# Performance work log

Hardware: AMD Instinct MI355X
Metric: run time of the kernel (lower is better)

## Reference

```python
import jax, jax.numpy as jnp
import numpy as np

LN_EPS = 1e-5

def setup_inputs() -> dict:
    key = jax.random.key(0)
    k1, k2, k3 = jax.random.split(key, 3)
    L, B, D = 2048, 8, 1024
    x = jax.random.normal(k1, (L, B, D), dtype=jnp.float32)
    c = jnp.zeros((B, D), dtype=jnp.float32)
    W = jax.random.normal(k2, (D, 3 * D), dtype=jnp.float32) * 0.02
    # bias init from _init_bias: u-bias 0, f-bias 0.5, r-bias 0
    b = jnp.concatenate([jnp.zeros(D), jnp.full((D,), 0.5), jnp.zeros(D)]).astype(jnp.float32)
    gamma = jnp.ones((D,), dtype=jnp.float32)
    beta = jnp.zeros((D,), dtype=jnp.float32)
    return {"x": x, "c": c, "W": W, "b": b, "gamma": gamma, "beta": beta}

def reference(x, c, W, b, gamma, beta):
    # LayerNorm over last dim
    mu = jnp.mean(x, axis=-1, keepdims=True)
    var = jnp.mean(jnp.square(x - mu), axis=-1, keepdims=True)
    x_norm = (x - mu) * jax.lax.rsqrt(var + LN_EPS) * gamma + beta
    # Fused u/f/r projection: [L,B,3D]
    ufr = jnp.einsum('lbd,de->lbe', x_norm, W) + b
    u, f, r = jnp.split(ufr, 3, axis=-1)
    f_gate = jax.nn.sigmoid(f)
    r_gate = jax.nn.sigmoid(r)
    # Linear recurrence c_t = f_t * c_{t-1} + (1-f_t) * u_t via scan over time
    def step(c_prev, fu):
        f_t, u_t = fu
        c_t = f_t * c_prev + (1.0 - f_t) * u_t
        return c_t, c_t
    last_c, c_stack = jax.lax.scan(step, c, (f_gate, u))
    hs = r_gate * jnp.tanh(c_stack) + (1.0 - r_gate) * x_norm
    return x + hs, last_c
```

## Files before the change

kernel.cpp:

```cpp
#include <hip/hip_runtime.h>
#include <hip/hip_bf16.h>


typedef unsigned short u16;
typedef __bf16 bf16x8 __attribute__((ext_vector_type(8)));
typedef float f32x4 __attribute__((ext_vector_type(4)));

#define L_DIM 2048
#define B_DIM 8
#define D_DIM 1024
#define M_DIM (L_DIM * B_DIM)
#define K_DIM D_DIM
#define N_DIM (3 * D_DIM)
#define NCH 32
#define CLEN (L_DIM / NCH)

__device__ __forceinline__ float bf2f(u16 h) {
    unsigned int u = ((unsigned int)h) << 16;
    float f;
    __builtin_memcpy(&f, &u, 4);
    return f;
}

__device__ __forceinline__ u16 f2bf(float f) {
    unsigned int u;
    __builtin_memcpy(&u, &f, 4);
    u = u + 0x7fff + ((u >> 16) & 1);
    return (u16)(u >> 16);
}

__device__ __forceinline__ void async16(void* lds, const void* g) {
    __builtin_amdgcn_global_load_lds(
        (const __attribute__((address_space(1))) void*)g,
        (__attribute__((address_space(3))) void*)lds, 16, 0, 0);
}

__global__ __launch_bounds__(256) void ln_kernel(const float* __restrict__ x,
                                                 const float* __restrict__ gamma,
                                                 const float* __restrict__ beta,
                                                 u16* __restrict__ xn) {
    int row = blockIdx.x;
    int tid = threadIdx.x;
    const float4* xr = (const float4*)(x + (size_t)row * D_DIM);
    float4 v = xr[tid];
    float s = v.x + v.y + v.z + v.w;
    float q = v.x * v.x + v.y * v.y + v.z * v.z + v.w * v.w;
    #pragma unroll
    for (int off = 32; off; off >>= 1) {
        s += __shfl_down(s, off);
        q += __shfl_down(q, off);
    }
    __shared__ float ss[4], qq[4];
    int lane = tid & 63, wv = tid >> 6;
    if (lane == 0) { ss[wv] = s; qq[wv] = q; }
    __syncthreads();
    s = ss[0] + ss[1] + ss[2] + ss[3];
    q = qq[0] + qq[1] + qq[2] + qq[3];
    float mu = s * (1.0f / D_DIM);
    float var = q * (1.0f / D_DIM) - mu * mu;
    float rs = rsqrtf(var + 1e-5f);
    float4 g = ((const float4*)gamma)[tid];
    float4 bt = ((const float4*)beta)[tid];
    ushort4 o;
    o.x = f2bf((v.x - mu) * rs * g.x + bt.x);
    o.y = f2bf((v.y - mu) * rs * g.y + bt.y);
    o.z = f2bf((v.z - mu) * rs * g.z + bt.z);
    o.w = f2bf((v.w - mu) * rs * g.w + bt.w);
    ((ushort4*)(xn + (size_t)row * D_DIM))[tid] = o;
}

__global__ __launch_bounds__(256) void wt_kernel(const float* __restrict__ W,
                                                 u16* __restrict__ Wt) {
    __shared__ float t[64][65];
    int k0 = blockIdx.x * 64;
    int n0 = blockIdx.y * 64;
    int col = threadIdx.x & 63;
    int rg4 = threadIdx.x >> 6;
    #pragma unroll
    for (int j = 0; j < 16; ++j) {
        int r = rg4 * 16 + j;
        t[r][col] = W[(size_t)(k0 + r) * N_DIM + n0 + col];
    }
    __syncthreads();
    #pragma unroll
    for (int j = 0; j < 16; ++j) {
        int nr = rg4 * 16 + j;
        Wt[(size_t)(n0 + nr) * K_DIM + k0 + col] = f2bf(t[col][nr]);
    }
}

__global__ __launch_bounds__(256) void gemm_kernel(const u16* __restrict__ A,
                                                   const u16* __restrict__ Bt,
                                                   const float* __restrict__ bias,
                                                   u16* __restrict__ uo,
                                                   u16* __restrict__ fo,
                                                   u16* __restrict__ ro) {
    __shared__ char lds[32768];
    char* ldsA = lds;
    char* ldsB = lds + 16384;
    int tid = threadIdx.x;
    int wave = tid >> 6, lane = tid & 63;
    int lm = lane & 15, lg = lane >> 4;
    int m0 = blockIdx.x * 128;
    int n0 = blockIdx.y * 128;
    int wm = wave >> 1, wn = wave & 1;

    f32x4 acc[4][4] = {};

    for (int kt = 0; kt < K_DIM / 64; ++kt) {
        int k0 = kt * 64;
        #pragma unroll
        for (int i = 0; i < 4; ++i) {
            int c = i * 256 + tid;
            int row = c >> 3;
            int colL = (c & 7) ^ (row & 7);
            const u16* ga = A + (size_t)(m0 + row) * K_DIM + k0 + colL * 8;
            async16(ldsA + i * 4096 + wave * 1024, ga);
            const u16* gb = Bt + (size_t)(n0 + row) * K_DIM + k0 + colL * 8;
            async16(ldsB + i * 4096 + wave * 1024, gb);
        }
        __syncthreads();
        #pragma unroll
        for (int kk = 0; kk < 2; ++kk) {
            bf16x8 av[4], bv[4];
            #pragma unroll
            for (int f = 0; f < 4; ++f) {
                int rowA = wm * 64 + f * 16 + lm;
                av[f] = *(const bf16x8*)(ldsA + rowA * 128 + (((kk * 4 + lg) ^ (rowA & 7)) << 4));
                int rowB = wn * 64 + f * 16 + lm;
                bv[f] = *(const bf16x8*)(ldsB + rowB * 128 + (((kk * 4 + lg) ^ (rowB & 7)) << 4));
            }
            #pragma unroll
            for (int fm = 0; fm < 4; ++fm)
                #pragma unroll
                for (int fn = 0; fn < 4; ++fn)
                    acc[fm][fn] = __builtin_amdgcn_mfma_f32_16x16x32_bf16(
                        av[fm], bv[fn], acc[fm][fn], 0, 0, 0);
        }
        __syncthreads();
    }

    int seg = n0 >> 10;
    u16* outp = (seg == 0) ? uo : ((seg == 1) ? fo : ro);
    #pragma unroll
    for (int fn = 0; fn < 4; ++fn) {
        #pragma unroll
        for (int fm = 0; fm < 4; ++fm) {
            int col = n0 + wn * 64 + fn * 16 + lm;
            int cm = col & 1023;
            float bb = bias[col];
            #pragma unroll
            for (int j = 0; j < 4; ++j) {
                int row = m0 + wm * 64 + fm * 16 + lg * 4 + j;
                float val = acc[fm][fn][j] + bb;
                if (seg != 0) val = 1.0f / (1.0f + __expf(-val));
                outp[(size_t)row * D_DIM + cm] = f2bf(val);
            }
        }
    }
}

__global__ __launch_bounds__(256) void scan1_kernel(const u16* __restrict__ fg,
                                                    const u16* __restrict__ u,
                                                    float* __restrict__ Aa,
                                                    float* __restrict__ Ss) {
    int ch = blockIdx.x;
    int bd = (blockIdx.y * 256 + threadIdx.x) * 2;
    int b = bd >> 10, d = bd & 1023;
    float a0 = 1.0f, a1 = 1.0f, s0 = 0.0f, s1 = 0.0f;
    for (int t = ch * CLEN; t < ch * CLEN + CLEN; ++t) {
        size_t idx = ((size_t)(t * B_DIM + b) << 10) + d;
        ushort2 f2 = *(const ushort2*)(fg + idx);
        ushort2 u2 = *(const ushort2*)(u + idx);
        float f0 = bf2f(f2.x), f1 = bf2f(f2.y);
        float v0 = bf2f(u2.x), v1 = bf2f(u2.y);
        s0 = f0 * s0 + (1.0f - f0) * v0;
        s1 = f1 * s1 + (1.0f - f1) * v1;
        a0 *= f0;
        a1 *= f1;
    }
    int o = ch * 8192 + bd;
    *(float2*)(Aa + o) = make_float2(a0, a1);
    *(float2*)(Ss + o) = make_float2(s0, s1);
}

__global__ __launch_bounds__(256) void scan2_kernel(const float* __restrict__ Aa,
                                                    const float* __restrict__ Ss,
                                                    const float* __restrict__ c0,
                                                    float* __restrict__ cs,
                                                    float* __restrict__ lastc) {
    int bd = blockIdx.x * 256 + threadIdx.x;
    float c = c0[bd];
    #pragma unroll 4
    for (int ch = 0; ch < NCH; ++ch) {
        cs[ch * 8192 + bd] = c;
        c = Aa[ch * 8192 + bd] * c + Ss[ch * 8192 + bd];
    }
    lastc[bd] = c;
}

__global__ __launch_bounds__(256) void scan3_kernel(const float* __restrict__ cs,
                                                    const u16* __restrict__ fg,
                                                    const u16* __restrict__ u,
                                                    const u16* __restrict__ rg,
                                                    const u16* __restrict__ xn,
                                                    const float* __restrict__ x,
                                                    float* __restrict__ out) {
    int ch = blockIdx.x;
    int bd = (blockIdx.y * 256 + threadIdx.x) * 2;
    int b = bd >> 10, d = bd & 1023;
    float c0v = cs[ch * 8192 + bd];
    float c1v = cs[ch * 8192 + bd + 1];
    for (int t = ch * CLEN; t < ch * CLEN + CLEN; ++t) {
        size_t idx = ((size_t)(t * B_DIM + b) << 10) + d;
        ushort2 f2 = *(const ushort2*)(fg + idx);
        ushort2 u2 = *(const ushort2*)(u + idx);
        ushort2 r2 = *(const ushort2*)(rg + idx);
        ushort2 n2 = *(const ushort2*)(xn + idx);
        float2 x2 = *(const float2*)(x + idx);
        float f0 = bf2f(f2.x), f1 = bf2f(f2.y);
        float v0 = bf2f(u2.x), v1 = bf2f(u2.y);
        float r0 = bf2f(r2.x), r1 = bf2f(r2.y);
        float n0 = bf2f(n2.x), n1 = bf2f(n2.y);
        c0v = f0 * c0v + (1.0f - f0) * v0;
        c1v = f1 * c1v + (1.0f - f1) * v1;
        float h0 = r0 * tanhf(c0v) + (1.0f - r0) * n0;
        float h1 = r1 * tanhf(c1v) + (1.0f - r1) * n1;
        *(float2*)(out + idx) = make_float2(x2.x + h0, x2.y + h1);
    }
}

extern "C" void kernel_launch(void* const* d_in, const int* in_sizes, int n_in,
                              void* d_out, int out_size, void* d_ws, size_t ws_size,
                              hipStream_t stream) {
    const float* x     = (const float*)d_in[0];
    const float* c0    = (const float*)d_in[1];
    const float* W     = (const float*)d_in[2];
    const float* b     = (const float*)d_in[3];
    const float* gamma = (const float*)d_in[4];
    const float* beta  = (const float*)d_in[5];
    float* out = (float*)d_out;
    float* lastc = out + (size_t)M_DIM * D_DIM;

    char* w = (char*)d_ws;
    u16* xn = (u16*)w;  w += (size_t)M_DIM * D_DIM * 2;
    u16* Wt = (u16*)w;  w += (size_t)N_DIM * K_DIM * 2;
    u16* ug = (u16*)w;  w += (size_t)M_DIM * D_DIM * 2;
    u16* fg = (u16*)w;  w += (size_t)M_DIM * D_DIM * 2;
    u16* rg = (u16*)w;  w += (size_t)M_DIM * D_DIM * 2;
    float* Aa = (float*)w; w += (size_t)NCH * 8192 * 4;
    float* Ss = (float*)w; w += (size_t)NCH * 8192 * 4;
    float* cs = (float*)w; w += (size_t)NCH * 8192 * 4;

    ln_kernel<<<M_DIM, 256, 0, stream>>>(x, gamma, beta, xn);
    wt_kernel<<<dim3(K_DIM / 64, N_DIM / 64), 256, 0, stream>>>(W, Wt);
    gemm_kernel<<<dim3(M_DIM / 128, N_DIM / 128), 256, 0, stream>>>(xn, Wt, b, ug, fg, rg);
    scan1_kernel<<<dim3(NCH, 16), 256, 0, stream>>>(fg, ug, Aa, Ss);
    scan2_kernel<<<32, 256, 0, stream>>>(Aa, Ss, c0, cs, lastc);
    scan3_kernel<<<dim3(NCH, 16), 256, 0, stream>>>(cs, fg, ug, rg, xn, x, out);
}
```

Measured before the change: 239.8 us.

## Rewrite GEMM as 256x256 tile with double-buffered LDS software pipeline

Replaces the 128x128 single-buffered GEMM with a 256x256 tile, 512-thread kernel that double-buffers A and B in 144KB of dynamic LDS. Asynchronous global-to-LDS loads for later k-tiles are interleaved with MFMA phases, using setprio, manual barriers and waitcnt. The goal is to hide load latency and raise data reuse per tile. In exchange it needs a large LDS allocation, limiting occupancy to one block per CU, and relies on fragile hand synchronisation.

```diff
diff --git a/kernel.cpp b/kernel.cpp
--- a/kernel.cpp
+++ b/kernel.cpp
@@ -14,6 +14,12 @@
 #define N_DIM (3 * D_DIM)
 #define NCH 32
 #define CLEN (L_DIM / NCH)
+#define NT (K_DIM / 64)
+
+#define LDS_A 0
+#define LDS_B 65536
+#define LDS_DUMMY 131072
+#define LDS_TOTAL 147456
 
 __device__ __forceinline__ float bf2f(u16 h) {
     unsigned int u = ((unsigned int)h) << 16;
@@ -89,75 +95,148 @@
     }
 }
 
-__global__ __launch_bounds__(256) void gemm_kernel(const u16* __restrict__ A,
-                                                   const u16* __restrict__ Bt,
-                                                   const float* __restrict__ bias,
-                                                   u16* __restrict__ uo,
-                                                   u16* __restrict__ fo,
-                                                   u16* __restrict__ ro) {
-    __shared__ char lds[32768];
-    char* ldsA = lds;
-    char* ldsB = lds + 16384;
-    int tid = threadIdx.x;
-    int wave = tid >> 6, lane = tid & 63;
-    int lm = lane & 15, lg = lane >> 4;
-    int m0 = blockIdx.x * 128;
-    int n0 = blockIdx.y * 128;
-    int wm = wave >> 1, wn = wave & 1;
-
-    f32x4 acc[4][4] = {};
-
-    for (int kt = 0; kt < K_DIM / 64; ++kt) {
-        int k0 = kt * 64;
-        #pragma unroll
-        for (int i = 0; i < 4; ++i) {
-            int c = i * 256 + tid;
-            int row = c >> 3;
-            int colL = (c & 7) ^ (row & 7);
-            const u16* ga = A + (size_t)(m0 + row) * K_DIM + k0 + colL * 8;
-            async16(ldsA + i * 4096 + wave * 1024, ga);
-            const u16* gb = Bt + (size_t)(n0 + row) * K_DIM + k0 + colL * 8;
-            async16(ldsB + i * 4096 + wave * 1024, gb);
-        }
-        __syncthreads();
-        #pragma unroll
-        for (int kk = 0; kk < 2; ++kk) {
-            bf16x8 av[4], bv[4];
-            #pragma unroll
-            for (int f = 0; f < 4; ++f) {
-                int rowA = wm * 64 + f * 16 + lm;
-                av[f] = *(const bf16x8*)(ldsA + rowA * 128 + (((kk * 4 + lg) ^ (rowA & 7)) << 4));
-                int rowB = wn * 64 + f * 16 + lm;
-                bv[f] = *(const bf16x8*)(ldsB + rowB * 128 + (((kk * 4 + lg) ^ (rowB & 7)) << 4));
-            }
-            #pragma unroll
-            for (int fm = 0; fm < 4; ++fm)
-                #pragma unroll
-                for (int fn = 0; fn < 4; ++fn)
-                    acc[fm][fn] = __builtin_amdgcn_mfma_f32_16x16x32_bf16(
-                        av[fm], bv[fn], acc[fm][fn], 0, 0, 0);
-        }
-        __syncthreads();
-    }
+__device__ __forceinline__ void stage_half(const u16* __restrict__ gsrc, int base0,
+                                           int t, int h, char* lds, int ldsOp,
+                                           int tid, int wave) {
+    int tc = (t < NT) ? t : 0;
+    int k0 = tc * 64;
+    char* dst0 = (t < NT) ? (lds + ldsOp + (t & 1) * 32768 + h * 16384)
+                          : (lds + LDS_DUMMY);
+    #pragma unroll
+    for (int s = 0; s < 2; ++s) {
+        int c = s * 512 + tid;
+        int row = h * 128 + (c >> 3);
+        int cc = (c & 7) ^ (row & 7);
+        async16(dst0 + s * 8192 + wave * 1024,
+                gsrc + (size_t)(base0 + row) * K_DIM + k0 + cc * 8);
+    }
+}
+
+__global__ __launch_bounds__(512, 2) void gemm_kernel(const u16* __restrict__ A,
+                                                      const u16* __restrict__ Bt,
+                                                      const float* __restrict__ bias,
+                                                      u16* __restrict__ uo,
+                                                      u16* __restrict__ fo,
+                                                      u16* __restrict__ ro) {
+    extern __shared__ char lds[];
+    const int tid = threadIdx.x;
+    const int wave = tid >> 6, lane = tid & 63;
+    const int lm = lane & 15, lg = lane >> 4;
+    const int wm = wave >> 2, wn = wave & 3;
+    const int m0 = blockIdx.x * 256;
+    const int n0 = blockIdx.y * 256;
+
+    f32x4 acc[8][4] = {};
+    bf16x8 av[4][2], aw[4][2], bv[4][2];
+
+#define LDA(dst, bb, mf0)                                                       \
+    do { _Pragma("unroll")                                                      \
+        for (int q = 0; q < 4; ++q) {                                           \
+            int row_ = wm * 128 + ((mf0) + q) * 16 + lm;                        \
+            const char* p_ = lds + LDS_A + (bb) * 32768 + row_ * 128;           \
+            _Pragma("unroll")                                                   \
+            for (int kk = 0; kk < 2; ++kk)                                      \
+                dst[q][kk] = *(const bf16x8*)(p_ + ((((kk << 2) | lg) ^ (row_ & 7)) << 4)); \
+        } } while (0)
+
+#define LDB(bb, kk)                                                             \
+    do { _Pragma("unroll")                                                      \
+        for (int nf = 0; nf < 4; ++nf) {                                        \
+            int row_ = wn * 64 + nf * 16 + lm;                                  \
+            bv[nf][kk] = *(const bf16x8*)(lds + LDS_B + (bb) * 32768 + row_ * 128 \
+                                          + ((((kk << 2) | lg) ^ (row_ & 7)) << 4)); \
+        } } while (0)
+
+#define MFMA16(r0, afr, kk)                                                     \
+    do { _Pragma("unroll")                                                      \
+        for (int q = 0; q < 4; ++q)                                             \
+            _Pragma("unroll")                                                   \
+            for (int nf = 0; nf < 4; ++nf)                                      \
+                acc[(r0) + q][nf] = __builtin_amdgcn_mfma_f32_16x16x32_bf16(    \
+                    afr[q][kk], bv[nf][kk], acc[(r0) + q][nf], 0, 0, 0);        \
+    } while (0)
+
+#define PH_SYNC()                                                               \
+    do { __builtin_amdgcn_s_barrier();                                          \
+         asm volatile("s_waitcnt lgkmcnt(0)");                                  \
+         __builtin_amdgcn_sched_barrier(0); } while (0)
+
+#define TILE_BODY(t, bb, last)                                                  \
+    do {                                                                        \
+                 \
+        LDA(av, bb, 0);                                                         \
+        LDB(bb, 0);                                                             \
+        stage_half(A, m0, (t) + 1, 0, lds, LDS_A, tid, wave);                   \
+        PH_SYNC();                                                              \
+        __builtin_amdgcn_s_setprio(1);                                          \
+        MFMA16(0, av, 0);                                                       \
+        __builtin_amdgcn_s_setprio(0);                                          \
+        __builtin_amdgcn_s_barrier();                                           \
+                                     \
+        LDB(bb, 1);                                                             \
+        stage_half(A, m0, (t) + 1, 1, lds, LDS_A, tid, wave);                   \
+        PH_SYNC();                                                              \
+        __builtin_amdgcn_s_setprio(1);                                          \
+        MFMA16(0, av, 1);                                                       \
+        __builtin_amdgcn_s_setprio(0);                                          \
+        __builtin_amdgcn_s_barrier();                                           \
+                                   \
+        LDA(aw, bb, 4);                                                         \
+        stage_half(Bt, n0, (t) + 2, 0, lds, LDS_B, tid, wave);                  \
+        PH_SYNC();                                                              \
+        __builtin_amdgcn_s_setprio(1);                                          \
+        MFMA16(4, aw, 0);                                                       \
+        __builtin_amdgcn_s_setprio(0);                                          \
+        __builtin_amdgcn_s_barrier();                                           \
+                         \
+        stage_half(Bt, n0, (t) + 2, 1, lds, LDS_B, tid, wave);                  \
+        __builtin_amdgcn_s_barrier();                                           \
+        __builtin_amdgcn_s_setprio(1);                                          \
+        MFMA16(4, aw, 1);                                                       \
+        __builtin_amdgcn_s_setprio(0);                                          \
+        if (!(last)) asm volatile("s_waitcnt vmcnt(4)" ::: "memory");           \
+        __builtin_amdgcn_s_barrier();                                           \
+    } while (0)
+
+    stage_half(A, m0, 0, 0, lds, LDS_A, tid, wave);
+    stage_half(A, m0, 0, 1, lds, LDS_A, tid, wave);
+    stage_half(Bt, n0, 0, 0, lds, LDS_B, tid, wave);
+    stage_half(Bt, n0, 0, 1, lds, LDS_B, tid, wave);
+    stage_half(Bt, n0, 1, 0, lds, LDS_B, tid, wave);
+    stage_half(Bt, n0, 1, 1, lds, LDS_B, tid, wave);
+    asm volatile("s_waitcnt vmcnt(4)" ::: "memory");
+    __builtin_amdgcn_s_barrier();
+
+    for (int t = 0; t < NT - 2; t += 2) {
+        TILE_BODY(t, 0, 0);
+        TILE_BODY(t + 1, 1, 0);
+    }
+    TILE_BODY(NT - 2, 0, 0);
+    TILE_BODY(NT - 1, 1, 1);
 
     int seg = n0 >> 10;
     u16* outp = (seg == 0) ? uo : ((seg == 1) ? fo : ro);
     #pragma unroll
-    for (int fn = 0; fn < 4; ++fn) {
+    for (int mf = 0; mf < 8; ++mf) {
         #pragma unroll
-        for (int fm = 0; fm < 4; ++fm) {
-            int col = n0 + wn * 64 + fn * 16 + lm;
+        for (int nf = 0; nf < 4; ++nf) {
+            int col = n0 + wn * 64 + nf * 16 + lm;
             int cm = col & 1023;
-            float bb = bias[col];
+            float bb2 = bias[col];
             #pragma unroll
             for (int j = 0; j < 4; ++j) {
-                int row = m0 + wm * 64 + fm * 16 + lg * 4 + j;
-                float val = acc[fm][fn][j] + bb;
+                int row = m0 + wm * 128 + mf * 16 + lg * 4 + j;
+                float val = acc[mf][nf][j] + bb2;
                 if (seg != 0) val = 1.0f / (1.0f + __expf(-val));
                 outp[(size_t)row * D_DIM + cm] = f2bf(val);
             }
         }
     }
+#undef LDA
+#undef LDB
+#undef MFMA16
+#undef PH_SYNC
+#undef TILE_BODY
 }
 
 __global__ __launch_bounds__(256) void scan1_kernel(const u16* __restrict__ fg,
@@ -252,9 +331,12 @@
     float* Ss = (float*)w; w += (size_t)NCH * 8192 * 4;
     float* cs = (float*)w; w += (size_t)NCH * 8192 * 4;
 
+    hipFuncSetAttribute(reinterpret_cast<const void*>(gemm_kernel),
+                        hipFuncAttributeMaxDynamicSharedMemorySize, LDS_TOTAL);
+
     ln_kernel<<<M_DIM, 256, 0, stream>>>(x, gamma, beta, xn);
     wt_kernel<<<dim3(K_DIM / 64, N_DIM / 64), 256, 0, stream>>>(W, Wt);
-    gemm_kernel<<<dim3(M_DIM / 128, N_DIM / 128), 256, 0, stream>>>(xn, Wt, b, ug, fg, rg);
+    gemm_kernel<<<dim3(M_DIM / 256, N_DIM / 256), 512, LDS_TOTAL, stream>>>(xn, Wt, b, ug, fg, rg);
     scan1_kernel<<<dim3(NCH, 16), 256, 0, stream>>>(fg, ug, Aa, Ss);
     scan2_kernel<<<32, 256, 0, stream>>>(Aa, Ss, c0, cs, lastc);
     scan3_kernel<<<dim3(NCH, 16), 256, 0, stream>>>(cs, fg, ug, rg, xn, x, out);
```

New measurement: 215.8 us. -10.0%, faster.
